# Optimization experiments

Measured on AMD Instinct MI355X. Metric: run time of the kernel, lower is better.

Reference implementation:

```python
import jax, jax.numpy as jnp
import numpy as np

B, N, H, F = 4, 256, 192, 64
SUP = 1.0  # ancestor_suppression_strength
EPS = 1e-6


def setup_inputs() -> dict:
    key = jax.random.key(0)
    ks = jax.random.split(key, 14)
    z = jax.random.normal(ks[0], (B, H), jnp.float32)
    # strictly-lower-triangular 0/1 parent (link) matrix: row t lists parents j < t
    tri = jnp.tril(jnp.ones((N, N), jnp.float32), -1)
    targets = (jax.random.uniform(ks[1], (B, N, N)) < 0.05).astype(jnp.float32) * tri

    def w(k, shape):
        fan_in = shape[0]
        return jax.random.normal(k, shape, jnp.float32) / jnp.sqrt(jnp.float32(fan_in))

    return {
        "z": z,
        "teacher_forcing_targets": targets,
        "W_init": w(ks[2], (H, H)), "b_init": jnp.zeros((H,), jnp.float32),
        "W_ih": w(ks[3], (H, 3 * H)), "W_hh": w(ks[4], (H, 3 * H)),
        "b_ih": jnp.zeros((3 * H,), jnp.float32), "b_hh": jnp.zeros((3 * H,), jnp.float32),
        "W1": w(ks[5], (3 * H, H)), "b1": jnp.zeros((H,), jnp.float32),
        "W2": w(ks[6], (H, 1)), "b2": jnp.zeros((1,), jnp.float32),
        "Wf": w(ks[7], (H, F)), "bf": jnp.zeros((F,), jnp.float32),
        "atom_count": N,
    }


def gru_cell(x, h, W_ih, W_hh, b_ih, b_hh):
    gx = x @ W_ih + b_ih
    gh = h @ W_hh + b_hh
    xr, xu, xn = jnp.split(gx, 3, axis=-1)
    hr, hu, hn = jnp.split(gh, 3, axis=-1)
    r = jax.nn.sigmoid(xr + hr)
    u = jax.nn.sigmoid(xu + hu)
    n = jnp.tanh(xn + r * hn)
    return (1.0 - u) * n + u * h


def reference(z, teacher_forcing_targets, W_init, b_init, W_ih, W_hh, b_ih, b_hh,
              W1, b1, W2, b2, Wf, bf, atom_count):
    b, n = teacher_forcing_targets.shape[0], teacher_forcing_targets.shape[1]
    h = z.shape[-1]
    idx = jnp.arange(n)

    # decoder_init: latent z -> hidden state of node 0
    h0 = jnp.tanh(z @ W_init + b_init)
    S0 = jnp.zeros((b, n, h), z.dtype).at[:, 0].set(h0)   # node states
    A0 = jnp.zeros((b, n, n), z.dtype)                    # ancestor indicator A[b,i,j]=1 iff j ancestor of i

    def step(carry, xs):
        S, A, ll = carry
        t, tgt = xs                                   # t scalar, tgt (B,N) = parents of node t
        mask = (idx < t).astype(S.dtype)              # existing nodes
        cnt = jnp.maximum(mask.sum(), 1.0)
        # mean-aggregation over existing node states -> GRU message
        m = (S * mask[None, :, None]).sum(axis=1) / cnt              # (B,H)
        h_prov = gru_cell(m, z, W_ih, W_hh, b_ih, b_hh)              # provisional state of new node
        # parent logits: MLP([h_new, h_existing, z]) per candidate parent
        feats = jnp.concatenate([
            jnp.broadcast_to(h_prov[:, None, :], S.shape), S,
            jnp.broadcast_to(z[:, None, :], S.shape)], axis=-1)      # (B,N,3H)
        logits = (jax.nn.relu(feats @ W1 + b1) @ W2 + b2)[..., 0]    # (B,N)
        # ancestor suppression: suppress j if j is already an ancestor of one of t's parents
        reach = jnp.einsum('bn,bnm->bm', tgt, A)
        anc = (reach > 0).astype(S.dtype)
        p = jax.nn.sigmoid(logits) * (1.0 - SUP * anc)
        p = jnp.clip(p, EPS, 1.0 - EPS)
        ll = ll + (mask[None, :] * (tgt * jnp.log(p) + (1.0 - tgt) * jnp.log1p(-p))).sum()
        # teacher forcing: commit parents, update new-node state from parent states
        deg = jnp.maximum(tgt.sum(axis=-1, keepdims=True), 1.0)
        msg = jnp.einsum('bn,bnh->bh', tgt, S) / deg
        h_new = gru_cell(msg, h_prov, W_ih, W_hh, b_ih, b_hh)
        S = jax.lax.dynamic_update_slice(S, h_new[:, None, :], (0, t, 0))
        row = jnp.minimum(tgt + anc, 1.0)             # ancestors(t) = parents U ancestors(parents)
        A = jax.lax.dynamic_update_slice(A, row[:, None, :], (0, t, 0))
        return (S, A, ll), None

    ts = jnp.arange(1, n)
    tgt_rows = jnp.swapaxes(teacher_forcing_targets[:, 1:, :], 0, 1)  # (N-1,B,N)
    (S, A, ll), _ = jax.lax.scan(step, (S0, A0, jnp.zeros((), z.dtype)), (ts, tgt_rows))

    L = teacher_forcing_targets            # teacher-forced link matrix
    node_features = S @ Wf + bf            # node_feature_decoder head
    return L, node_features, ll
```

## Files before the change

### kernel.cpp

```cpp
#include <hip/hip_runtime.h>
#include <stdint.h>

#define B_ 4
#define N_ 256
#define H_ 192
#define H3_ 576
#define F_ 64

#define H0_OFF   0u
#define ZC_OFF   1024u
#define HL_OFF   2048u
#define SL_OFF   395264u
#define AN_OFF   788480u
#define TG_OFF   796672u
#define PL_OFF   804864u
#define PC_OFF   870400u
#define DG_OFF   871424u
#define D_OFF    872448u
#define G_OFF    1462272u
#define C_OFF    1658880u
#define FHL_OFF  1855488u
#define FSL_OFF  2248704u
#define XC_OFF   2641920u

#define AN64 (AN_OFF/2)
#define TG64 (TG_OFF/2)

#define NF_OUT 262144u
#define LL_OUT 327680u

__device__ __forceinline__ float sigm_(float x){ return 1.0f/(1.0f + __expf(-x)); }
__device__ __forceinline__ float tanh_(float x){
  float ax = fabsf(x);
  float e = __expf(-2.0f*ax);
  float t = (1.0f - e)/(1.0f + e);
  return x < 0.0f ? -t : t;
}

__device__ __forceinline__ void st_mall_(uint32_t* p, unsigned long long u){
  __hip_atomic_store((unsigned long long*)p, u, __ATOMIC_RELAXED, __HIP_MEMORY_SCOPE_AGENT);
}
__device__ __forceinline__ unsigned long long ld_mall_(const uint32_t* p){
  return __hip_atomic_load((const unsigned long long*)p, __ATOMIC_RELAXED, __HIP_MEMORY_SCOPE_AGENT);
}
__device__ __forceinline__ unsigned long long ld_nt_(const uint32_t* p){
  unsigned long long v;
  asm volatile("global_load_dwordx2 %0, %1, off nt\n\t"
               "s_waitcnt vmcnt(0)"
               : "=v"(v) : "v"(p) : "memory");
  return v;
}
__device__ __forceinline__ void pub_(uint32_t* fp, uint32_t* mp, float v, uint32_t tag){
  unsigned long long u = ((unsigned long long)tag<<32) | (unsigned long long)__float_as_uint(v);
  __hip_atomic_store((unsigned long long*)fp, u, __ATOMIC_RELAXED, __HIP_MEMORY_SCOPE_WORKGROUP);
  st_mall_(mp, u);
}
__device__ __forceinline__ float pollH_(const uint32_t* fp, const uint32_t* mp, uint32_t tag){
  unsigned long long x;
  for(;;){
    x = ld_nt_(fp);
    if ((uint32_t)(x>>32) != tag){
      unsigned long long m = ld_mall_(mp);
      if ((uint32_t)(m>>32) == tag) x = m;
    }
    if (__all((int)((uint32_t)(x>>32) == tag))) break;
  }
  return __uint_as_float((uint32_t)x);
}
__device__ __forceinline__ void bar_(){
  asm volatile("s_waitcnt lgkmcnt(0)" ::: "memory");
  __builtin_amdgcn_s_barrier();
  asm volatile("" ::: "memory");
}

__global__ void __launch_bounds__(192) k_pre1(const float* __restrict__ z,
    const float* __restrict__ Winit, const float* __restrict__ binit,
    const float* __restrict__ W1, const float* __restrict__ b1,
    const float* __restrict__ tgt, float* ws, float* out)
{
  int bx = blockIdx.x, b = blockIdx.y, tid = threadIdx.x;
  if (bx == N_){
    __shared__ float zs[H_];
    zs[tid] = z[b*H_ + tid];
    __syncthreads();
    float a0=0.f, a1=0.f;
    for (int k=0;k<H_;k++){
      float zv = zs[k];
      a0 += zv * Winit[(size_t)k*H_ + tid];
      a1 += zv * W1[(size_t)(2*H_ + k)*H_ + tid];
    }
    ws[H0_OFF + b*H_ + tid] = tanh_(a0 + binit[tid]);
    ws[ZC_OFF + b*H_ + tid] = a1 + b1[tid];
    if (b==0 && tid==0) out[LL_OUT] = 0.0f;
    return;
  }
  if (tid >= 64) return;
  int t = bx, lane = tid;
  uint32_t* wsu = (uint32_t*)ws;
  unsigned long long* ws64 = (unsigned long long*)ws;
  const float* row = tgt + ((size_t)(b*N_) + t)*N_;
  uint8_t* pl = ((uint8_t*)&wsu[PL_OFF]) + (size_t)(b*N_ + t)*N_;
  int cnt = 0;
  #pragma unroll
  for (int m=0;m<4;m++){
    float v = row[m*64 + lane];
    bool p = (v != 0.0f);
    unsigned long long bw = __ballot(p);
    if (lane == 0) ws64[TG64 + (size_t)(b*N_+t)*4 + m] = bw;
    if (p){
      int pos = cnt + (int)__popcll(bw & ((1ULL<<lane)-1ULL));
      pl[pos] = (uint8_t)(m*64 + lane);
    }
    cnt += (int)__popcll(bw);
  }
  if (lane == 0){
    wsu[PC_OFF + b*N_ + t] = (uint32_t)cnt;
    ws[DG_OFF + b*N_ + t] = 1.0f / fmaxf((float)cnt, 1.0f);
  }
}

__global__ void __launch_bounds__(512, 2) k_pass1(const float* __restrict__ z,
    const float* __restrict__ Wih, const float* __restrict__ Whh,
    const float* __restrict__ bih_g, const float* __restrict__ bhh_g,
    float* ws)
{
  int bx = blockIdx.x;
  int b = bx & 7;
  if (b >= B_) return;
  int blk = bx >> 3;
  int tid = threadIdx.x;
  const int e  = tid >> 3;
  const int kc = tid & 7;
  const int E  = blk*64 + e;

  float* wsf = ws;
  uint32_t* wsu = (uint32_t*)ws;
  unsigned long long* ws64 = (unsigned long long*)ws;

  __shared__ __align__(16) float sh[H_];
  __shared__ __align__(16) float ss[H_];
  __shared__ float sDG[N_], sTF1[N_];
  __shared__ uint32_t sPC[N_];
  __shared__ unsigned long long sAB[N_][4];

  {
    float v = wsf[H0_OFF + b*H_ + E];
    if (kc == 0)
      pub_(&wsu[FSL_OFF + (unsigned)(b*N_)*384u + 2u*(unsigned)E],
           &wsu[SL_OFF  + (unsigned)(b*N_)*384u + 2u*(unsigned)E], v, 1u);
    if (kc == 1) ss[E] = v;
  }

  for (int i = tid; i < N_; i += 512){
    sDG[i] = wsf[DG_OFF + b*N_ + i];
    sPC[i] = wsu[PC_OFF + b*N_ + i];
    float f1 = 0.f;
    if (i >= 1){
      unsigned long long w1 = ws64[TG64 + (size_t)(b*N_+i)*4 + ((i-1)>>6)];
      f1 = (float)((w1 >> ((i-1)&63)) & 1ULL);
    }
    sTF1[i] = f1;
  }
  if (blk == 0 && tid >= 192 && tid < 196) sAB[0][tid-192] = 0ULL;

  float rwih[3][24], rwhh[3][24], rbih[3], rbhh[3], rghz[3];
  #pragma unroll
  for (int g=0; g<3; g++){
    int col = g*H_ + E;
    #pragma unroll
    for (int i=0;i<24;i++){
      rwih[g][i] = Wih[(size_t)(kc*24+i)*H3_ + col];
      rwhh[g][i] = Whh[(size_t)(kc*24+i)*H3_ + col];
    }
    rbih[g] = bih_g[col];
    rbhh[g] = bhh_g[col];
  }
  {
    float a0=0.f,a1=0.f,a2=0.f;
    #pragma unroll
    for (int i=0;i<24;i++){
      float zv = z[b*H_ + kc*24 + i];
      a0 += zv*rwhh[0][i]; a1 += zv*rwhh[1][i]; a2 += zv*rwhh[2][i];
    }
    #pragma unroll
    for (int m=1;m<8;m<<=1){
      a0 += __shfl_xor(a0,m); a1 += __shfl_xor(a1,m); a2 += __shfl_xor(a2,m);
    }
    rghz[0]=a0+rbhh[0]; rghz[1]=a1+rbhh[1]; rghz[2]=a2+rbhh[2];
  }
  float zreg = z[b*H_ + E];

  __syncthreads();
  if (tid < 128){
    int j = (tid < blk*64) ? tid : tid + 64;
    ss[j] = pollH_(&wsu[FSL_OFF + (unsigned)(b*N_)*384u + 2u*(unsigned)j],
                   &wsu[SL_OFF  + (unsigned)(b*N_)*384u + 2u*(unsigned)j], 1u);
  }
  __syncthreads();

  float q0=0.f, q1=0.f, q2=0.f;
  const uint8_t* plbase = ((const uint8_t*)&wsu[PL_OFF]) + (size_t)(b*N_)*N_;
  float* Dbase = wsf + D_OFF + (size_t)((b*3+blk)*N_)*H_;

  for (int t=1; t<N_; t++){
    const uint32_t tagH = (uint32_t)(t+1);
    float d0=0.f,d1=0.f,d2=0.f;
    #pragma unroll
    for (int c=0;c<6;c++){
      float4 v4 = *(const float4*)&ss[kc*24 + c*4];
      float xx0=v4.x, xx1=v4.y, xx2=v4.z, xx3=v4.w;
      d0 += xx0*rwih[0][c*4+0]; d1 += xx0*rwih[1][c*4+0]; d2 += xx0*rwih[2][c*4+0];
      d0 += xx1*rwih[0][c*4+1]; d1 += xx1*rwih[1][c*4+1]; d2 += xx1*rwih[2][c*4+1];
      d0 += xx2*rwih[0][c*4+2]; d1 += xx2*rwih[1][c*4+2]; d2 += xx2*rwih[2][c*4+2];
      d0 += xx3*rwih[0][c*4+3]; d1 += xx3*rwih[1][c*4+3]; d2 += xx3*rwih[2][c*4+3];
    }
    #pragma unroll
    for (int m=1;m<8;m<<=1){
      d0 += __shfl_xor(d0,m); d1 += __shfl_xor(d1,m); d2 += __shfl_xor(d2,m);
    }
    q0 += d0; q1 += d1; q2 += d2;
    float invt = 1.0f/(float)t;
    float r = sigm_(q0*invt + rbih[0] + rghz[0]);
    float u = sigm_(q1*invt + rbih[1] + rghz[1]);
    float n = tanh_(q2*invt + rbih[2] + r*rghz[2]);
    float hp = (1.0f-u)*n + u*zreg;
    if (kc == 0){
      pub_(&wsu[FHL_OFF + (unsigned)(b*N_+t)*384u + 2u*(unsigned)E],
           &wsu[HL_OFF  + (unsigned)(b*N_+t)*384u + 2u*(unsigned)E], hp, tagH);
      float* Dr = Dbase + (size_t)(t-1)*H_;
      Dr[e] = d0; Dr[64+e] = d1; Dr[128+e] = d2;
    }
    if (kc == 1) sh[E] = hp;
    float ga0=0.f, ga1=0.f, ga2=0.f;
    {
      int pc = (int)sPC[t];
      const uint8_t* pl = plbase + (size_t)t*N_;
      for (int i=kc; i<pc; i+=8){
        int p = pl[i];
        if (p == t-1) continue;
        const float* Dp = Dbase + (size_t)p*H_;
        ga0 += Dp[e]; ga1 += Dp[64+e]; ga2 += Dp[128+e];
      }
    }
    #pragma unroll
    for (int m=1;m<8;m<<=1){
      ga0 += __shfl_xor(ga0,m); ga1 += __shfl_xor(ga1,m); ga2 += __shfl_xor(ga2,m);
    }
    if (tid < 128){
      int j = (tid < blk*64) ? tid : tid + 64;
      sh[j] = pollH_(&wsu[FHL_OFF + (unsigned)(b*N_+t)*384u + 2u*(unsigned)j],
                     &wsu[HL_OFF  + (unsigned)(b*N_+t)*384u + 2u*(unsigned)j], tagH);
    } else if (blk == 0 && tid >= 192 && tid < 208){
      int lane16 = tid - 192;
      int ip = lane16 >> 2, w = lane16 & 3;
      int pc = (int)sPC[t];
      const uint8_t* pl = plbase + (size_t)t*N_;
      unsigned long long acc = 0ULL;
      for (int i=ip; i<pc; i+=4) acc |= sAB[pl[i]][w];
      acc |= __shfl_xor(acc, 4);
      acc |= __shfl_xor(acc, 8);
      if (ip == 0){
        ws64[AN64 + (size_t)(b*N_+t)*4 + w] = acc;
        sAB[t][w] = acc | ws64[TG64 + (size_t)(b*N_+t)*4 + w];
      }
    }
    bar_();
    float y0=0.f,y1=0.f,y2=0.f;
    #pragma unroll
    for (int c=0;c<6;c++){
      float4 v4 = *(const float4*)&sh[kc*24 + c*4];
      float xx0=v4.x, xx1=v4.y, xx2=v4.z, xx3=v4.w;
      y0 += xx0*rwhh[0][c*4+0]; y1 += xx0*rwhh[1][c*4+0]; y2 += xx0*rwhh[2][c*4+0];
      y0 += xx1*rwhh[0][c*4+1]; y1 += xx1*rwhh[1][c*4+1]; y2 += xx1*rwhh[2][c*4+1];
      y0 += xx2*rwhh[0][c*4+2]; y1 += xx2*rwhh[1][c*4+2]; y2 += xx2*rwhh[2][c*4+2];
      y0 += xx3*rwhh[0][c*4+3]; y1 += xx3*rwhh[1][c*4+3]; y2 += xx3*rwhh[2][c*4+3];
    }
    #pragma unroll
    for (int m=1;m<8;m<<=1){
      y0 += __shfl_xor(y0,m); y1 += __shfl_xor(y1,m); y2 += __shfl_xor(y2,m);
    }
    float dginv = sDG[t], tf1 = sTF1[t];
    float gxa = (ga0 + tf1*d0)*dginv + rbih[0];
    float gxb = (ga1 + tf1*d1)*dginv + rbih[1];
    float gxc = (ga2 + tf1*d2)*dginv + rbih[2];
    float r2 = sigm_(gxa + y0 + rbhh[0]);
    float u2 = sigm_(gxb + y1 + rbhh[1]);
    float n2 = tanh_(gxc + r2*(y2 + rbhh[2]));
    float hn = (1.0f-u2)*n2 + u2*hp;
    if (kc == 0)
      pub_(&wsu[FSL_OFF + (unsigned)(b*N_+t)*384u + 2u*(unsigned)E],
           &wsu[SL_OFF  + (unsigned)(b*N_+t)*384u + 2u*(unsigned)E], hn, tagH);
    if (kc == 1) ss[E] = hn;
    if (tid < 128){
      int j = (tid < blk*64) ? tid : tid + 64;
      ss[j] = pollH_(&wsu[FSL_OFF + (unsigned)(b*N_+t)*384u + 2u*(unsigned)j],
                     &wsu[SL_OFF  + (unsigned)(b*N_+t)*384u + 2u*(unsigned)j], tagH);
    }
    bar_();
  }
}

__global__ void k_p2a(const float* __restrict__ W1, const float* __restrict__ Wf,
    const float* __restrict__ bf, float* ws, float* out)
{
  int j = blockIdx.x, b = blockIdx.y, tid = threadIdx.x;
  __shared__ float srow[H_], hrow[H_];
  __shared__ float nfp[3][F_];
  srow[tid] = ws[SL_OFF + (unsigned)(b*N_+j)*384u + 2u*tid];
  hrow[tid] = ws[HL_OFF + (unsigned)(b*N_+j)*384u + 2u*tid];
  __syncthreads();
  float accG = 0.f, accC = 0.f;
  for (int k=0;k<H_;k++){
    float sv = srow[k], hv = hrow[k];
    accG += sv * W1[(size_t)(H_+k)*H_ + tid];
    accC += hv * W1[(size_t)k*H_ + tid];
  }
  ws[G_OFF + ((size_t)b*H_ + tid)*N_ + j] = accG;
  ws[C_OFF + (size_t)(b*N_+j)*H_ + tid] = accC + ws[ZC_OFF + b*H_ + tid];
  int f = tid & 63, kp = tid >> 6;
  float a = 0.f;
  for (int i=0;i<64;i++){ int k = kp*64 + i; a += srow[k]*Wf[(size_t)k*F_ + f]; }
  nfp[kp][f] = a;
  __syncthreads();
  if (tid < F_) out[NF_OUT + (size_t)(b*N_+j)*F_ + tid] = nfp[0][tid]+nfp[1][tid]+nfp[2][tid] + bf[tid];
}

__global__ void __launch_bounds__(256) k_p2b(const float* __restrict__ W2,
    const float* __restrict__ b2p, float* ws, float* out)
{
  int t = blockIdx.x + 1, b = blockIdx.y;
  int tid = threadIdx.x; int lane = tid & 63; int wv = tid >> 6;
  __shared__ float cv[H_], w2s[H_];
  __shared__ float wsum[4];
  unsigned long long* ws64 = (unsigned long long*)ws;
  if (tid < H_){
    cv[tid] = ws[C_OFF + (size_t)(b*N_+t)*H_ + tid];
    w2s[tid] = W2[tid];
  }
  __syncthreads();
  float acc = 0.f;
  if (tid < t){
    const float* GT = ws + G_OFF + (size_t)b*H_*N_;
    float a = 0.f;
    for (int k=0;k<H_;k++) a += fmaxf(cv[k] + GT[(size_t)k*N_ + tid], 0.f) * w2s[k];
    float logit = a + b2p[0];
    float pp = 1.0f/(1.0f+__expf(-logit));
    unsigned long long an = ws64[AN64 + (size_t)(b*N_+t)*4 + (tid>>6)];
    unsigned long long tg = ws64[TG64 + (size_t)(b*N_+t)*4 + (tid>>6)];
    float anc = (float)((an >> (tid&63)) & 1ULL);
    pp = pp * (1.0f - anc);
    pp = fminf(fmaxf(pp, 1e-6f), 1.0f - 1e-6f);
    int tgb = (int)((tg >> (tid&63)) & 1ULL);
    acc = tgb ? logf(pp) : log1pf(-pp);
  }
  #pragma unroll
  for (int m=32;m>=1;m>>=1) acc += __shfl_xor(acc, m);
  if (lane == 0) wsum[wv] = acc;
  __syncthreads();
  if (tid == 0) atomicAdd(out + LL_OUT, wsum[0]+wsum[1]+wsum[2]+wsum[3]);
}

extern "C" void kernel_launch(void* const* d_in, const int* in_sizes, int n_in,
                              void* d_out, int out_size, void* d_ws, size_t ws_size,
                              hipStream_t stream) {
  (void)in_sizes; (void)n_in; (void)out_size; (void)ws_size;
  const float* z     = (const float*)d_in[0];
  const float* tgt   = (const float*)d_in[1];
  const float* Winit = (const float*)d_in[2];
  const float* binit = (const float*)d_in[3];
  const float* Wih   = (const float*)d_in[4];
  const float* Whh   = (const float*)d_in[5];
  const float* bih   = (const float*)d_in[6];
  const float* bhh   = (const float*)d_in[7];
  const float* W1    = (const float*)d_in[8];
  const float* b1    = (const float*)d_in[9];
  const float* W2    = (const float*)d_in[10];
  const float* b2    = (const float*)d_in[11];
  const float* Wf    = (const float*)d_in[12];
  const float* bf    = (const float*)d_in[13];
  float* out = (float*)d_out;
  float* ws  = (float*)d_ws;

  hipMemcpyAsync(d_out, d_in[1], (size_t)B_*N_*N_*sizeof(float), hipMemcpyDeviceToDevice, stream);

  k_pre1<<<dim3(N_+1, B_), dim3(192), 0, stream>>>(z, Winit, binit, W1, b1, tgt, ws, out);
  k_pass1<<<dim3(24), dim3(512), 0, stream>>>(z, Wih, Whh, bih, bhh, ws);
  k_p2a<<<dim3(N_, B_), dim3(H_), 0, stream>>>(W1, Wf, bf, ws, out);
  k_p2b<<<dim3(N_-1, B_), dim3(256), 0, stream>>>(W2, b2, ws, out);
}
```

Baseline: 910.9 us.

## Repartition recurrent GRU pass across six blocks with split-K partial exchange

The sequential recurrence kernel changes from 3 blocks per batch, each owning 64 output columns, to 6 blocks per batch. Each block owns 32 hidden units, keeps its weight slices in dynamic LDS, and exchanges split-K partial products of the new state times W_ih through tagged global slots. Ancestor-mask propagation moves into a separate k_anc kernel, and z·W_hh is precomputed in k_pre1. The aim is to cut per-step cross-block polling and per-block work on the serial critical path, at the cost of more inter-block messages per step and more barriers.

Result: slower. 2.254 ms (+147.5%).

```diff
diff --git a/kernel.cpp b/kernel.cpp
--- a/kernel.cpp
+++ b/kernel.cpp
@@ -6,28 +6,51 @@
 #define H_ 192
 #define H3_ 576
 #define F_ 64
+#define NBLK 6
+#define OWNE 32
+#define OWNC 96
 
 #define H0_OFF   0u
 #define ZC_OFF   1024u
-#define HL_OFF   2048u
-#define SL_OFF   395264u
-#define AN_OFF   788480u
-#define TG_OFF   796672u
-#define PL_OFF   804864u
-#define PC_OFF   870400u
-#define DG_OFF   871424u
-#define D_OFF    872448u
-#define G_OFF    1462272u
-#define C_OFF    1658880u
-#define FHL_OFF  1855488u
-#define FSL_OFF  2248704u
-#define XC_OFF   2641920u
+#define GZ_OFF   2048u
+#define SG_OFF   4608u
+#define HPG_OFF  201216u
+#define AN_OFF   397824u
+#define TG_OFF   406016u
+#define PL_OFF   414208u
+#define PC_OFF   479744u
+#define DG_OFF   480768u
+#define D_OFF    481792u
+#define G_OFF    1071616u
+#define C_OFF    1268224u
+#define FDP_OFF  1464832u
+#define MDP_OFF  1520128u
 
 #define AN64 (AN_OFF/2)
 #define TG64 (TG_OFF/2)
+#define FDP64 (FDP_OFF/2)
+#define MDP64 (MDP_OFF/2)
+#define MOFF64 ((MDP_OFF-FDP_OFF)/2)
 
 #define NF_OUT 262144u
 #define LL_OUT 327680u
+
+#define L_WIH   0u
+#define L_WHH   18464u
+#define L_Q     37088u
+#define L_GZ    37664u
+#define L_BIH   38240u
+#define L_HP    38816u
+#define L_ZF    39008u
+#define L_DOWN  39200u
+#define L_YGA   39296u
+#define L_GAA   39392u
+#define L_BHH   39488u
+#define L_SSO   39584u
+#define L_SPC   39616u
+#define L_STF   39872u
+#define SMEM_WORDS 39880u
+#define SMEM_BYTES (SMEM_WORDS*4u)
 
 __device__ __forceinline__ float sigm_(float x){ return 1.0f/(1.0f + __expf(-x)); }
 __device__ __forceinline__ float tanh_(float x){
@@ -37,35 +60,29 @@
   return x < 0.0f ? -t : t;
 }
 
-__device__ __forceinline__ void st_mall_(uint32_t* p, unsigned long long u){
-  __hip_atomic_store((unsigned long long*)p, u, __ATOMIC_RELAXED, __HIP_MEMORY_SCOPE_AGENT);
-}
-__device__ __forceinline__ unsigned long long ld_mall_(const uint32_t* p){
-  return __hip_atomic_load((const unsigned long long*)p, __ATOMIC_RELAXED, __HIP_MEMORY_SCOPE_AGENT);
-}
-__device__ __forceinline__ unsigned long long ld_nt_(const uint32_t* p){
-  unsigned long long v;
-  asm volatile("global_load_dwordx2 %0, %1, off nt\n\t"
-               "s_waitcnt vmcnt(0)"
-               : "=v"(v) : "v"(p) : "memory");
-  return v;
-}
-__device__ __forceinline__ void pub_(uint32_t* fp, uint32_t* mp, float v, uint32_t tag){
-  unsigned long long u = ((unsigned long long)tag<<32) | (unsigned long long)__float_as_uint(v);
-  __hip_atomic_store((unsigned long long*)fp, u, __ATOMIC_RELAXED, __HIP_MEMORY_SCOPE_WORKGROUP);
-  st_mall_(mp, u);
-}
-__device__ __forceinline__ float pollH_(const uint32_t* fp, const uint32_t* mp, uint32_t tag){
-  unsigned long long x;
-  for(;;){
-    x = ld_nt_(fp);
-    if ((uint32_t)(x>>32) != tag){
-      unsigned long long m = ld_mall_(mp);
-      if ((uint32_t)(m>>32) == tag) x = m;
-    }
-    if (__all((int)((uint32_t)(x>>32) == tag))) break;
-  }
-  return __uint_as_float((uint32_t)x);
+__device__ __forceinline__ void st_mall_(unsigned long long* p, unsigned long long u){
+  __hip_atomic_store(p, u, __ATOMIC_RELAXED, __HIP_MEMORY_SCOPE_AGENT);
+}
+__device__ __forceinline__ unsigned long long ld_mall_(const unsigned long long* p){
+  return __hip_atomic_load(p, __ATOMIC_RELAXED, __HIP_MEMORY_SCOPE_AGENT);
+}
+__device__ __forceinline__ void st_fast_(unsigned long long* p, unsigned long long u){
+  __hip_atomic_store(p, u, __ATOMIC_RELAXED, __HIP_MEMORY_SCOPE_WORKGROUP);
+}
+__device__ __forceinline__ void ld_nt5_(const unsigned long long* p0, const unsigned long long* p1,
+    const unsigned long long* p2, const unsigned long long* p3, const unsigned long long* p4,
+    unsigned long long& x0, unsigned long long& x1, unsigned long long& x2,
+    unsigned long long& x3, unsigned long long& x4){
+  asm volatile(
+    "global_load_dwordx2 %0, %5, off nt\n\t"
+    "global_load_dwordx2 %1, %6, off nt\n\t"
+    "global_load_dwordx2 %2, %7, off nt\n\t"
+    "global_load_dwordx2 %3, %8, off nt\n\t"
+    "global_load_dwordx2 %4, %9, off nt\n\t"
+    "s_waitcnt vmcnt(0)"
+    : "=&v"(x0),"=&v"(x1),"=&v"(x2),"=&v"(x3),"=&v"(x4)
+    : "v"(p0),"v"(p1),"v"(p2),"v"(p3),"v"(p4)
+    : "memory");
 }
 __device__ __forceinline__ void bar_(){
   asm volatile("s_waitcnt lgkmcnt(0)" ::: "memory");
@@ -76,6 +93,7 @@
 __global__ void __launch_bounds__(192) k_pre1(const float* __restrict__ z,
     const float* __restrict__ Winit, const float* __restrict__ binit,
     const float* __restrict__ W1, const float* __restrict__ b1,
+    const float* __restrict__ Whh, const float* __restrict__ bhh,
     const float* __restrict__ tgt, float* ws, float* out)
 {
   int bx = blockIdx.x, b = blockIdx.y, tid = threadIdx.x;
@@ -91,6 +109,13 @@
     }
     ws[H0_OFF + b*H_ + tid] = tanh_(a0 + binit[tid]);
     ws[ZC_OFF + b*H_ + tid] = a1 + b1[tid];
+    #pragma unroll
+    for (int g=0; g<3; g++){
+      int c = g*H_ + tid;
+      float a = 0.f;
+      for (int k=0;k<H_;k++) a += zs[k]*Whh[(size_t)k*H3_ + c];
+      ws[GZ_OFF + b*H3_ + c] = a + bhh[c];
+    }
     if (b==0 && tid==0) out[LL_OUT] = 0.0f;
     return;
   }
@@ -119,182 +144,221 @@
   }
 }
 
-__global__ void __launch_bounds__(512, 2) k_pass1(const float* __restrict__ z,
+__global__ void __launch_bounds__(64) k_anc(float* ws)
+{
+  int b = blockIdx.x, lane = threadIdx.x;
+  uint32_t* wsu = (uint32_t*)ws;
+  unsigned long long* ws64 = (unsigned long long*)ws;
+  __shared__ unsigned long long AB[N_][4];
+  if (lane < 4) AB[0][lane] = 0ULL;
+  __syncthreads();
+  const uint8_t* plb = ((const uint8_t*)&wsu[PL_OFF]) + (size_t)(b*N_)*N_;
+  for (int t=1; t<N_; t++){
+    if (lane < 16){
+      int ip = lane>>2, w = lane&3;
+      int pc = (int)wsu[PC_OFF + b*N_ + t];
+      const uint8_t* pl = plb + (size_t)t*N_;
+      unsigned long long acc = 0ULL;
+      for (int i=ip;i<pc;i+=4) acc |= AB[pl[i]][w];
+      acc |= __shfl_xor(acc, 4);
+      acc |= __shfl_xor(acc, 8);
+      if (ip == 0){
+        ws64[AN64 + (size_t)(b*N_+t)*4 + w] = acc;
+        AB[t][w] = acc | ws64[TG64 + (size_t)(b*N_+t)*4 + w];
+      }
+    }
+    __syncthreads();
+  }
+}
+
+__global__ void __launch_bounds__(512, 1) k_pass1(const float* __restrict__ z,
     const float* __restrict__ Wih, const float* __restrict__ Whh,
     const float* __restrict__ bih_g, const float* __restrict__ bhh_g,
     float* ws)
 {
+  extern __shared__ __align__(16) char smem_[];
+  float* L = (float*)smem_;
+  uint32_t* Lu = (uint32_t*)smem_;
+
   int bx = blockIdx.x;
-  int b = bx & 7;
-  if (b >= B_) return;
-  int blk = bx >> 3;
+  int b   = bx & 3;
+  int blk = bx >> 2;
   int tid = threadIdx.x;
-  const int e  = tid >> 3;
-  const int kc = tid & 7;
-  const int E  = blk*64 + e;
 
   float* wsf = ws;
   uint32_t* wsu = (uint32_t*)ws;
   unsigned long long* ws64 = (unsigned long long*)ws;
 
-  __shared__ __align__(16) float sh[H_];
-  __shared__ __align__(16) float ss[H_];
-  __shared__ float sDG[N_], sTF1[N_];
-  __shared__ uint32_t sPC[N_];
-  __shared__ unsigned long long sAB[N_][4];
-
-  {
-    float v = wsf[H0_OFF + b*H_ + E];
-    if (kc == 0)
-      pub_(&wsu[FSL_OFF + (unsigned)(b*N_)*384u + 2u*(unsigned)E],
-           &wsu[SL_OFF  + (unsigned)(b*N_)*384u + 2u*(unsigned)E], v, 1u);
-    if (kc == 1) ss[E] = v;
-  }
-
-  for (int i = tid; i < N_; i += 512){
-    sDG[i] = wsf[DG_OFF + b*N_ + i];
-    sPC[i] = wsu[PC_OFF + b*N_ + i];
-    float f1 = 0.f;
-    if (i >= 1){
-      unsigned long long w1 = ws64[TG64 + (size_t)(b*N_+i)*4 + ((i-1)>>6)];
-      f1 = (float)((w1 >> ((i-1)&63)) & 1ULL);
-    }
-    sTF1[i] = f1;
-  }
-  if (blk == 0 && tid >= 192 && tid < 196) sAB[0][tid-192] = 0ULL;
-
-  float rwih[3][24], rwhh[3][24], rbih[3], rbhh[3], rghz[3];
+  for (int idx = tid; idx < OWNE*H3_; idx += 512){
+    int k = idx / H3_, c = idx % H3_;
+    L[L_WIH + k*577 + c] = Wih[(size_t)(OWNE*blk + k)*H3_ + c];
+  }
+  for (int idx = tid; idx < H_*OWNC; idx += 512){
+    int k = idx / OWNC, oc = idx % OWNC;
+    int g = oc >> 5, jj = oc & 31;
+    int gcol = g*H_ + OWNE*blk + jj;
+    L[L_WHH + k*97 + oc] = Whh[(size_t)k*H3_ + gcol];
+  }
+  for (int c = tid; c < H3_; c += 512){
+    L[L_Q + c]   = 0.0f;
+    L[L_GZ + c]  = wsf[GZ_OFF + b*H3_ + c];
+    L[L_BIH + c] = bih_g[c];
+  }
+  for (int e = tid; e < H_; e += 512) L[L_ZF + e] = z[b*H_ + e];
+  for (int oc = tid; oc < OWNC; oc += 512){
+    int g = oc >> 5, jj = oc & 31;
+    L[L_BHH + oc] = bhh_g[g*H_ + OWNE*blk + jj];
+  }
+  for (int i = tid; i < N_; i += 512) Lu[L_SPC + i] = wsu[PC_OFF + b*N_ + i];
+  if (tid < OWNE){
+    float h0 = wsf[H0_OFF + b*H_ + OWNE*blk + tid];
+    L[L_SSO + tid] = h0;
+    wsf[SG_OFF + (size_t)(b*N_)*H_ + OWNE*blk + tid] = h0;
+  }
+  __syncthreads();
+
+  const int c1 = tid;
+  const int c2 = (tid < 64) ? tid + 512 : -1;
+  int cm1 = c1 % H_;
+  const int own1 = ((cm1 >> 5) == blk);
+  const int oc1 = (c1/H_)*OWNE + (cm1 & 31);
+  int own2 = 0, oc2 = 0;
+  if (c2 >= 0){
+    int cm2 = c2 % H_;
+    own2 = ((cm2 >> 5) == blk);
+    oc2 = (c2/H_)*OWNE + (cm2 & 31);
+  }
+  unsigned long long* ownF1 = ws64 + FDP64 + (size_t)((b*NBLK+blk)*2)*H3_ + c1;
+  unsigned long long* ownF2 = (c2>=0) ? ws64 + FDP64 + (size_t)((b*NBLK+blk)*2)*H3_ + c2 : (unsigned long long*)0;
+  unsigned long long* pb1[5];
+  unsigned long long* pb2[5];
   #pragma unroll
-  for (int g=0; g<3; g++){
-    int col = g*H_ + E;
-    #pragma unroll
-    for (int i=0;i<24;i++){
-      rwih[g][i] = Wih[(size_t)(kc*24+i)*H3_ + col];
-      rwhh[g][i] = Whh[(size_t)(kc*24+i)*H3_ + col];
-    }
-    rbih[g] = bih_g[col];
-    rbhh[g] = bhh_g[col];
-  }
-  {
-    float a0=0.f,a1=0.f,a2=0.f;
-    #pragma unroll
-    for (int i=0;i<24;i++){
-      float zv = z[b*H_ + kc*24 + i];
-      a0 += zv*rwhh[0][i]; a1 += zv*rwhh[1][i]; a2 += zv*rwhh[2][i];
-    }
-    #pragma unroll
-    for (int m=1;m<8;m<<=1){
-      a0 += __shfl_xor(a0,m); a1 += __shfl_xor(a1,m); a2 += __shfl_xor(a2,m);
-    }
-    rghz[0]=a0+rbhh[0]; rghz[1]=a1+rbhh[1]; rghz[2]=a2+rbhh[2];
-  }
-  float zreg = z[b*H_ + E];
-
-  __syncthreads();
-  if (tid < 128){
-    int j = (tid < blk*64) ? tid : tid + 64;
-    ss[j] = pollH_(&wsu[FSL_OFF + (unsigned)(b*N_)*384u + 2u*(unsigned)j],
-                   &wsu[SL_OFF  + (unsigned)(b*N_)*384u + 2u*(unsigned)j], 1u);
-  }
-  __syncthreads();
-
-  float q0=0.f, q1=0.f, q2=0.f;
+  for (int f=0; f<5; f++){
+    int fb = (f < blk) ? f : f+1;
+    pb1[f] = ws64 + FDP64 + (size_t)((b*NBLK+fb)*2)*H3_ + c1;
+    pb2[f] = (c2>=0) ? ws64 + FDP64 + (size_t)((b*NBLK+fb)*2)*H3_ + c2 : (unsigned long long*)0;
+  }
+  float* Dglob = wsf + D_OFF + (size_t)((b*NBLK+blk)*N_)*OWNC;
   const uint8_t* plbase = ((const uint8_t*)&wsu[PL_OFF]) + (size_t)(b*N_)*N_;
-  float* Dbase = wsf + D_OFF + (size_t)((b*3+blk)*N_)*H_;
+  const int ocE = tid >> 2, kcE = tid & 3;
 
   for (int t=1; t<N_; t++){
     const uint32_t tagH = (uint32_t)(t+1);
-    float d0=0.f,d1=0.f,d2=0.f;
+    const int parO = (t & 1) * H3_;
+    float dp1 = 0.f, dp2 = 0.f;
     #pragma unroll
-    for (int c=0;c<6;c++){
-      float4 v4 = *(const float4*)&ss[kc*24 + c*4];
-      float xx0=v4.x, xx1=v4.y, xx2=v4.z, xx3=v4.w;
-      d0 += xx0*rwih[0][c*4+0]; d1 += xx0*rwih[1][c*4+0]; d2 += xx0*rwih[2][c*4+0];
-      d0 += xx1*rwih[0][c*4+1]; d1 += xx1*rwih[1][c*4+1]; d2 += xx1*rwih[2][c*4+1];
-      d0 += xx2*rwih[0][c*4+2]; d1 += xx2*rwih[1][c*4+2]; d2 += xx2*rwih[2][c*4+2];
-      d0 += xx3*rwih[0][c*4+3]; d1 += xx3*rwih[1][c*4+3]; d2 += xx3*rwih[2][c*4+3];
-    }
-    #pragma unroll
-    for (int m=1;m<8;m<<=1){
-      d0 += __shfl_xor(d0,m); d1 += __shfl_xor(d1,m); d2 += __shfl_xor(d2,m);
-    }
-    q0 += d0; q1 += d1; q2 += d2;
-    float invt = 1.0f/(float)t;
-    float r = sigm_(q0*invt + rbih[0] + rghz[0]);
-    float u = sigm_(q1*invt + rbih[1] + rghz[1]);
-    float n = tanh_(q2*invt + rbih[2] + r*rghz[2]);
-    float hp = (1.0f-u)*n + u*zreg;
-    if (kc == 0){
-      pub_(&wsu[FHL_OFF + (unsigned)(b*N_+t)*384u + 2u*(unsigned)E],
-           &wsu[HL_OFF  + (unsigned)(b*N_+t)*384u + 2u*(unsigned)E], hp, tagH);
-      float* Dr = Dbase + (size_t)(t-1)*H_;
-      Dr[e] = d0; Dr[64+e] = d1; Dr[128+e] = d2;
-    }
-    if (kc == 1) sh[E] = hp;
-    float ga0=0.f, ga1=0.f, ga2=0.f;
+    for (int k=0; k<OWNE; k++){
+      float sv = L[L_SSO + k];
+      dp1 += sv * L[L_WIH + k*577 + c1];
+      if (c2 >= 0) dp2 += sv * L[L_WIH + k*577 + c2];
+    }
     {
-      int pc = (int)sPC[t];
-      const uint8_t* pl = plbase + (size_t)t*N_;
-      for (int i=kc; i<pc; i+=8){
-        int p = pl[i];
-        if (p == t-1) continue;
-        const float* Dp = Dbase + (size_t)p*H_;
-        ga0 += Dp[e]; ga1 += Dp[64+e]; ga2 += Dp[128+e];
-      }
-    }
-    #pragma unroll
-    for (int m=1;m<8;m<<=1){
-      ga0 += __shfl_xor(ga0,m); ga1 += __shfl_xor(ga1,m); ga2 += __shfl_xor(ga2,m);
-    }
-    if (tid < 128){
-      int j = (tid < blk*64) ? tid : tid + 64;
-      sh[j] = pollH_(&wsu[FHL_OFF + (unsigned)(b*N_+t)*384u + 2u*(unsigned)j],
-                     &wsu[HL_OFF  + (unsigned)(b*N_+t)*384u + 2u*(unsigned)j], tagH);
-    } else if (blk == 0 && tid >= 192 && tid < 208){
-      int lane16 = tid - 192;
-      int ip = lane16 >> 2, w = lane16 & 3;
-      int pc = (int)sPC[t];
-      const uint8_t* pl = plbase + (size_t)t*N_;
-      unsigned long long acc = 0ULL;
-      for (int i=ip; i<pc; i+=4) acc |= sAB[pl[i]][w];
-      acc |= __shfl_xor(acc, 4);
-      acc |= __shfl_xor(acc, 8);
-      if (ip == 0){
-        ws64[AN64 + (size_t)(b*N_+t)*4 + w] = acc;
-        sAB[t][w] = acc | ws64[TG64 + (size_t)(b*N_+t)*4 + w];
-      }
+      unsigned long long u1 = ((unsigned long long)tagH<<32) | (unsigned long long)__float_as_uint(dp1);
+      st_fast_(ownF1 + parO, u1);
+      st_mall_(ownF1 + parO + MOFF64, u1);
+      if (c2 >= 0){
+        unsigned long long u2 = ((unsigned long long)tagH<<32) | (unsigned long long)__float_as_uint(dp2);
+        st_fast_(ownF2 + parO, u2);
+        st_mall_(ownF2 + parO + MOFF64, u2);
+      }
+    }
+    float sum1 = dp1, sum2 = dp2;
+    unsigned got = (c2 >= 0) ? 0u : 0x3E0u;
+    int it = 0;
+    while (got != 0x3FFu){
+      unsigned long long x0,x1,x2,x3,x4;
+      ld_nt5_(pb1[0]+parO, pb1[1]+parO, pb1[2]+parO, pb1[3]+parO, pb1[4]+parO, x0,x1,x2,x3,x4);
+      unsigned long long xa[5] = {x0,x1,x2,x3,x4};
+      #pragma unroll
+      for (int f=0; f<5; f++){
+        if (!((got>>f)&1u) && (uint32_t)(xa[f]>>32) == tagH){
+          sum1 += __uint_as_float((uint32_t)xa[f]); got |= 1u<<f;
+        }
+      }
+      if (c2 >= 0){
+        ld_nt5_(pb2[0]+parO, pb2[1]+parO, pb2[2]+parO, pb2[3]+parO, pb2[4]+parO, x0,x1,x2,x3,x4);
+        unsigned long long xb[5] = {x0,x1,x2,x3,x4};
+        #pragma unroll
+        for (int f=0; f<5; f++){
+          if (!((got>>(5+f))&1u) && (uint32_t)(xb[f]>>32) == tagH){
+            sum2 += __uint_as_float((uint32_t)xb[f]); got |= 1u<<(5+f);
+          }
+        }
+      }
+      if (got == 0x3FFu) break;
+      if ((it & 3) == 2){
+        #pragma unroll
+        for (int f=0; f<5; f++){
+          if (!((got>>f)&1u)){
+            unsigned long long m = ld_mall_(pb1[f]+parO+MOFF64);
+            if ((uint32_t)(m>>32) == tagH){ sum1 += __uint_as_float((uint32_t)m); got |= 1u<<f; }
+          }
+          if (c2 >= 0 && !((got>>(5+f))&1u)){
+            unsigned long long m = ld_mall_(pb2[f]+parO+MOFF64);
+            if ((uint32_t)(m>>32) == tagH){ sum2 += __uint_as_float((uint32_t)m); got |= 1u<<(5+f); }
+          }
+        }
+      }
+      if (++it > 12) __builtin_amdgcn_s_sleep(2);
+    }
+    L[L_Q + c1] += sum1;
+    if (own1){ L[L_DOWN + oc1] = sum1; Dglob[(size_t)(t-1)*OWNC + oc1] = sum1; }
+    if (c2 >= 0){
+      L[L_Q + c2] += sum2;
+      if (own2){ L[L_DOWN + oc2] = sum2; Dglob[(size_t)(t-1)*OWNC + oc2] = sum2; }
+    }
+    if (tid == 511){
+      unsigned long long w1 = ws64[TG64 + (size_t)(b*N_+t)*4 + ((t-1)>>6)];
+      L[L_STF] = (float)((w1 >> ((t-1)&63)) & 1ULL);
     }
     bar_();
-    float y0=0.f,y1=0.f,y2=0.f;
-    #pragma unroll
-    for (int c=0;c<6;c++){
-      float4 v4 = *(const float4*)&sh[kc*24 + c*4];
-      float xx0=v4.x, xx1=v4.y, xx2=v4.z, xx3=v4.w;
-      y0 += xx0*rwhh[0][c*4+0]; y1 += xx0*rwhh[1][c*4+0]; y2 += xx0*rwhh[2][c*4+0];
-      y0 += xx1*rwhh[0][c*4+1]; y1 += xx1*rwhh[1][c*4+1]; y2 += xx1*rwhh[2][c*4+1];
-      y0 += xx2*rwhh[0][c*4+2]; y1 += xx2*rwhh[1][c*4+2]; y2 += xx2*rwhh[2][c*4+2];
-      y0 += xx3*rwhh[0][c*4+3]; y1 += xx3*rwhh[1][c*4+3]; y2 += xx3*rwhh[2][c*4+3];
-    }
-    #pragma unroll
-    for (int m=1;m<8;m<<=1){
-      y0 += __shfl_xor(y0,m); y1 += __shfl_xor(y1,m); y2 += __shfl_xor(y2,m);
-    }
-    float dginv = sDG[t], tf1 = sTF1[t];
-    float gxa = (ga0 + tf1*d0)*dginv + rbih[0];
-    float gxb = (ga1 + tf1*d1)*dginv + rbih[1];
-    float gxc = (ga2 + tf1*d2)*dginv + rbih[2];
-    float r2 = sigm_(gxa + y0 + rbhh[0]);
-    float u2 = sigm_(gxb + y1 + rbhh[1]);
-    float n2 = tanh_(gxc + r2*(y2 + rbhh[2]));
-    float hn = (1.0f-u2)*n2 + u2*hp;
-    if (kc == 0)
-      pub_(&wsu[FSL_OFF + (unsigned)(b*N_+t)*384u + 2u*(unsigned)E],
-           &wsu[SL_OFF  + (unsigned)(b*N_+t)*384u + 2u*(unsigned)E], hn, tagH);
-    if (kc == 1) ss[E] = hn;
-    if (tid < 128){
-      int j = (tid < blk*64) ? tid : tid + 64;
-      ss[j] = pollH_(&wsu[FSL_OFF + (unsigned)(b*N_+t)*384u + 2u*(unsigned)j],
-                     &wsu[SL_OFF  + (unsigned)(b*N_+t)*384u + 2u*(unsigned)j], tagH);
+    if (tid < H_){
+      float invt = 1.0f/(float)t;
+      int e = tid;
+      float r = sigm_(L[L_Q+e]*invt       + L[L_BIH+e]       + L[L_GZ+e]);
+      float u = sigm_(L[L_Q+H_+e]*invt    + L[L_BIH+H_+e]    + L[L_GZ+H_+e]);
+      float n = tanh_(L[L_Q+2*H_+e]*invt  + L[L_BIH+2*H_+e]  + r*L[L_GZ+2*H_+e]);
+      L[L_HP + e] = (1.0f-u)*n + u*L[L_ZF+e];
+    }
+    bar_();
+    if (tid < 384){
+      float y = 0.f;
+      const int k0 = kcE*48;
+      #pragma unroll
+      for (int k=0; k<48; k++) y += L[L_HP + k0 + k] * L[L_WHH + (k0+k)*97 + ocE];
+      float ga = 0.f;
+      {
+        int pc = (int)Lu[L_SPC + t];
+        const uint8_t* pl = plbase + (size_t)t*N_;
+        for (int i=kcE; i<pc; i+=4){
+          int p = pl[i];
+          if (p == t-1) continue;
+          ga += Dglob[(size_t)p*OWNC + ocE];
+        }
+      }
+      y  += __shfl_xor(y, 1);  y  += __shfl_xor(y, 2);
+      ga += __shfl_xor(ga, 1); ga += __shfl_xor(ga, 2);
+      if (kcE == 0){ L[L_YGA + ocE] = y; L[L_GAA + ocE] = ga; }
+    } else if (blk == 0){
+      for (int e = tid-384; e < H_; e += 128)
+        wsf[HPG_OFF + (size_t)(b*N_+t)*H_ + e] = L[L_HP + e];
+    }
+    bar_();
+    if (tid < OWNE){
+      int jj = tid;
+      int pc = (int)Lu[L_SPC + t];
+      float dgv = 1.0f / fmaxf((float)pc, 1.0f);
+      float tf1 = L[L_STF];
+      int gcb = OWNE*blk + jj;
+      float gr = (L[L_GAA+jj]      + tf1*L[L_DOWN+jj])      * dgv + L[L_BIH + gcb];
+      float gu = (L[L_GAA+32+jj]   + tf1*L[L_DOWN+32+jj])   * dgv + L[L_BIH + H_ + gcb];
+      float gn = (L[L_GAA+64+jj]   + tf1*L[L_DOWN+64+jj])   * dgv + L[L_BIH + 2*H_ + gcb];
+      float r2 = sigm_(gr + L[L_YGA+jj]    + L[L_BHH+jj]);
+      float u2 = sigm_(gu + L[L_YGA+32+jj] + L[L_BHH+32+jj]);
+      float n2 = tanh_(gn + r2*(L[L_YGA+64+jj] + L[L_BHH+64+jj]));
+      float hn = (1.0f-u2)*n2 + u2*L[L_HP + gcb];
+      L[L_SSO + jj] = hn;
+      wsf[SG_OFF + (size_t)(b*N_+t)*H_ + gcb] = hn;
     }
     bar_();
   }
@@ -306,8 +370,8 @@
   int j = blockIdx.x, b = blockIdx.y, tid = threadIdx.x;
   __shared__ float srow[H_], hrow[H_];
   __shared__ float nfp[3][F_];
-  srow[tid] = ws[SL_OFF + (unsigned)(b*N_+j)*384u + 2u*tid];
-  hrow[tid] = ws[HL_OFF + (unsigned)(b*N_+j)*384u + 2u*tid];
+  srow[tid] = ws[SG_OFF + (size_t)(b*N_+j)*H_ + tid];
+  hrow[tid] = ws[HPG_OFF + (size_t)(b*N_+j)*H_ + tid];
   __syncthreads();
   float accG = 0.f, accC = 0.f;
   for (int k=0;k<H_;k++){
@@ -381,10 +445,18 @@
   float* out = (float*)d_out;
   float* ws  = (float*)d_ws;
 
+  static int smem_set = 0;
+  if (!smem_set){
+    hipFuncSetAttribute(reinterpret_cast<const void*>(&k_pass1),
+                        hipFuncAttributeMaxDynamicSharedMemorySize, (int)SMEM_BYTES);
+    smem_set = 1;
+  }
+
   hipMemcpyAsync(d_out, d_in[1], (size_t)B_*N_*N_*sizeof(float), hipMemcpyDeviceToDevice, stream);
 
-  k_pre1<<<dim3(N_+1, B_), dim3(192), 0, stream>>>(z, Winit, binit, W1, b1, tgt, ws, out);
-  k_pass1<<<dim3(24), dim3(512), 0, stream>>>(z, Wih, Whh, bih, bhh, ws);
+  k_pre1<<<dim3(N_+1, B_), dim3(192), 0, stream>>>(z, Winit, binit, W1, b1, Whh, bhh, tgt, ws, out);
+  k_anc<<<dim3(B_), dim3(64), 0, stream>>>(ws);
+  k_pass1<<<dim3(B_*NBLK), dim3(512), SMEM_BYTES, stream>>>(z, Wih, Whh, bih, bhh, ws);
   k_p2a<<<dim3(N_, B_), dim3(H_), 0, stream>>>(W1, Wf, bf, ws, out);
   k_p2b<<<dim3(N_-1, B_), dim3(256), 0, stream>>>(W2, b2, ws, out);
 }
```
